# Performance work log

Measured on AMD Instinct MI355X. Metric: run time of the kernel, lower is better.

The kernel has to match this reference:

```python
import jax, jax.numpy as jnp
import numpy as np

B, N, K = 64, 128, 12
D_ATOM, D_NBR, D_NEW = 256, 320, 256
H, DK = 8, 32  # D_NEW = H * DK
LN_EPS = 1e-5
NEG_INF = -1e9


def setup_inputs() -> dict:
    key = jax.random.key(0)
    ks = jax.random.split(key, 10)
    atom_feature = jax.random.normal(ks[0], (B, N, D_ATOM), jnp.float32)
    atom_neighbor_feature = jax.random.normal(ks[1], (B, N, K, D_NBR), jnp.float32)
    # valid-neighbor masks from random neighbor counts in [1, K]
    counts = jax.random.randint(ks[2], (B, N), 1, K + 1)
    valid = (jnp.arange(K)[None, None, :] < counts[:, :, None]).astype(jnp.float32)
    atom_attend_mask = valid[..., None]                      # (B,N,K,1), 1=real neighbor
    atom_softmax_mask = (1.0 - valid[..., None]) * NEG_INF   # (B,N,K,1), additive
    # parameters
    s = 1.0 / np.sqrt(D_ATOM)
    W_atom = jax.random.uniform(ks[3], (D_ATOM, D_NEW), jnp.float32, -s, s)
    b_atom = jnp.zeros((D_NEW,), jnp.float32)
    s2 = 1.0 / np.sqrt(D_NBR)
    W_nbr = jax.random.uniform(ks[4], (D_NBR, D_NEW), jnp.float32, -s2, s2)
    b_nbr = jnp.zeros((D_NEW,), jnp.float32)
    s3 = 1.0 / np.sqrt(DK)
    w_align = jax.random.uniform(ks[5], (DK, 1), jnp.float32, -s3, s3)
    b_align = jnp.zeros((1,), jnp.float32)
    ln_gamma = jnp.ones((D_NEW,), jnp.float32)
    ln_beta = jnp.zeros((D_NEW,), jnp.float32)
    return dict(atom_feature=atom_feature, atom_neighbor_feature=atom_neighbor_feature,
                atom_softmax_mask=atom_softmax_mask, atom_attend_mask=atom_attend_mask,
                W_atom=W_atom, b_atom=b_atom, W_nbr=W_nbr, b_nbr=b_nbr,
                w_align=w_align, b_align=b_align, ln_gamma=ln_gamma, ln_beta=ln_beta)


def reference(atom_feature, atom_neighbor_feature, atom_softmax_mask, atom_attend_mask,
              W_atom, b_atom, W_nbr, b_nbr, w_align, b_align, ln_gamma, ln_beta):
    # dropout is identity at eval time
    h = atom_feature @ W_atom + b_atom                    # (B,N,D_NEW)
    e = atom_neighbor_feature @ W_nbr + b_nbr             # (B,N,K,D_NEW)
    h = h.reshape(B, N, 1, H, DK)                         # broadcast over K
    e = e.reshape(B, N, K, H, DK)
    # GATv2: act(h_i + e_j) then per-head linear score
    feat = jax.nn.leaky_relu(h + e)                       # slope 0.01 == torch default
    score = feat @ w_align + b_align                      # (B,N,K,H,1)
    score = score + atom_softmax_mask[:, :, :, None, :]   # additive -inf on pad
    attn = jax.nn.softmax(score, axis=2)                  # softmax over neighbors K
    attn = attn * atom_attend_mask[:, :, :, None, :]
    ctx = jnp.sum(attn * e, axis=2).reshape(B, N, H * DK)  # (B,N,D_NEW)
    # LayerNorm
    mu = jnp.mean(ctx, axis=-1, keepdims=True)
    xc = ctx - mu
    var = jnp.mean(xc * xc, axis=-1, keepdims=True)
    return xc * jax.lax.rsqrt(var + LN_EPS) * ln_gamma + ln_beta
```

## Files before the change

kernel.cpp:

```cpp
#include <hip/hip_runtime.h>

#define KN 12
#define DNBR 320
#define DNEW 256
#define BN_TOT 8192
#define ATB 2
#define NKS_E 10
#define NKS_H 8
#define ASTR_E 328
#define ASTR_H 264

typedef short bf8_t __attribute__((ext_vector_type(8)));
typedef float f32x4 __attribute__((ext_vector_type(4)));
typedef unsigned short us8 __attribute__((ext_vector_type(8)));
using u16 = unsigned short;
using u32 = unsigned int;

__device__ __forceinline__ u16 f2bf(float f) {
    u32 x = __float_as_uint(f);
    return (u16)((x + 0x7fffu + ((x >> 16) & 1u)) >> 16);
}

__device__ __forceinline__ us8 pack8(float4 a, float4 b) {
    us8 v;
    v[0] = f2bf(a.x); v[1] = f2bf(a.y); v[2] = f2bf(a.z); v[3] = f2bf(a.w);
    v[4] = f2bf(b.x); v[5] = f2bf(b.y); v[6] = f2bf(b.z); v[7] = f2bf(b.w);
    return v;
}

__global__ __launch_bounds__(256) void build_b2(
    const float* __restrict__ Wn, const float* __restrict__ Wa,
    u16* __restrict__ B2)
{
    int tile = blockIdx.x * 4 + (threadIdx.x >> 6);
    int l = threadIdx.x & 63;
    int q = l >> 4, m = l & 15;
    us8 v;
    if (tile < 160) {
        int ks = tile >> 4, nt = tile & 15;
        int col = nt * 16 + m;
#pragma unroll
        for (int e = 0; e < 8; e++)
            v[e] = f2bf(Wn[(ks * 32 + q * 8 + e) * DNEW + col]);
    } else {
        int tt = tile - 160;
        int ks = tt >> 4, nt = tt & 15;
        int col = nt * 16 + m;
#pragma unroll
        for (int e = 0; e < 8; e++)
            v[e] = f2bf(Wa[(ks * 32 + q * 8 + e) * DNEW + col]);
    }
    *(us8*)&B2[(size_t)tile * 512 + l * 8] = v;
}

__global__ __launch_bounds__(256, 4) void fused_all(
    const float* __restrict__ atomf, const float* __restrict__ nbrf,
    const float* __restrict__ smaskg, const float* __restrict__ amaskg,
    const float* __restrict__ ba, const u16* __restrict__ B2,
    const float* __restrict__ bnb, const float* __restrict__ walg,
    const float* __restrict__ balg, const float* __restrict__ gam,
    const float* __restrict__ bet, float* __restrict__ out)
{
    __shared__ u16 A_e[32 * ASTR_E];
    __shared__ u16 A_h[16 * ASTR_H];
    __shared__ float h_l[ATB][256];
    __shared__ float ctx_l[ATB][256];
    __shared__ float s_l[ATB][8][12];
    __shared__ float attnm_l[ATB][8][16];
    __shared__ float bnb_l[256], ba_l[256], wal_l[32];
    __shared__ float smask_l[ATB * 12], amask_l[ATB * 12];
    __shared__ float red_l[ATB][8];

    const int t = threadIdx.x;
    const int l = t & 63, w = t >> 6, q = l >> 4, m = l & 15;
    const int a0 = blockIdx.x * ATB;

    bnb_l[t] = bnb[t];
    ba_l[t] = ba[t];
    if (t < 32) wal_l[t] = walg[t];
    else if (t >= 32 && t < 56) smask_l[t - 32] = smaskg[(size_t)a0 * KN + (t - 32)];
    else if (t >= 64 && t < 88) amask_l[t - 64] = amaskg[(size_t)a0 * KN + (t - 64)];

    const float* nbase = nbrf + (size_t)a0 * (KN * DNBR);
    for (int i = t; i < 960; i += 256) {
        float4 v0 = *(const float4*)(nbase + i * 8);
        float4 v1 = *(const float4*)(nbase + i * 8 + 4);
        int at = i / 480, rem = i - at * 480;
        int row = rem / 40, c8 = rem - row * 40;
        *(us8*)&A_e[(at * 16 + row) * ASTR_E + c8 * 8] = pack8(v0, v1);
    }
    for (int i = t; i < 328; i += 256) {
        int at = i / 164, rem = i - at * 164;
        int rr = rem / 41, c8 = rem - rr * 41;
        us8 z = {0, 0, 0, 0, 0, 0, 0, 0};
        *(us8*)&A_e[(at * 16 + 12 + rr) * ASTR_E + c8 * 8] = z;
    }
    if (t < 64) {
        int at = t >> 5, c8 = t & 31;
        const float* s = atomf + (size_t)(a0 + at) * DNEW + c8 * 8;
        *(us8*)&A_h[at * ASTR_H + c8 * 8] = pack8(*(const float4*)s, *(const float4*)(s + 4));
    }
    for (int i = t; i < 462; i += 256) {
        int rr = i / 33, c8 = i - rr * 33;
        us8 z = {0, 0, 0, 0, 0, 0, 0, 0};
        *(us8*)&A_h[(2 + rr) * ASTR_H + c8 * 8] = z;
    }
    __syncthreads();

    f32x4 acc_e[ATB][4];
    f32x4 acc_h[4];
#pragma unroll
    for (int at = 0; at < ATB; at++)
#pragma unroll
        for (int j = 0; j < 4; j++) acc_e[at][j] = (f32x4){0.f, 0.f, 0.f, 0.f};
#pragma unroll
    for (int j = 0; j < 4; j++) acc_h[j] = (f32x4){0.f, 0.f, 0.f, 0.f};

    for (int ks = 0; ks < NKS_E; ks++) {
        bf8_t af0 = *(bf8_t*)&A_e[(0 * 16 + m) * ASTR_E + ks * 32 + q * 8];
        bf8_t af1 = *(bf8_t*)&A_e[(1 * 16 + m) * ASTR_E + ks * 32 + q * 8];
        bf8_t bf[4];
#pragma unroll
        for (int j = 0; j < 4; j++)
            bf[j] = *(const bf8_t*)&B2[((size_t)(ks * 16 + w * 4 + j) * 64 + l) * 8];
#pragma unroll
        for (int j = 0; j < 4; j++) {
            acc_e[0][j] = __builtin_amdgcn_mfma_f32_16x16x32_bf16(af0, bf[j], acc_e[0][j], 0, 0, 0);
            acc_e[1][j] = __builtin_amdgcn_mfma_f32_16x16x32_bf16(af1, bf[j], acc_e[1][j], 0, 0, 0);
        }
    }
    for (int ks = 0; ks < NKS_H; ks++) {
        bf8_t af = *(bf8_t*)&A_h[m * ASTR_H + ks * 32 + q * 8];
#pragma unroll
        for (int j = 0; j < 4; j++) {
            bf8_t bfj = *(const bf8_t*)&B2[((size_t)(160 + ks * 16 + w * 4 + j) * 64 + l) * 8];
            acc_h[j] = __builtin_amdgcn_mfma_f32_16x16x32_bf16(af, bfj, acc_h[j], 0, 0, 0);
        }
    }
    if (q == 0) {
#pragma unroll
        for (int j = 0; j < 4; j++) {
            int col = w * 64 + j * 16 + m;
            h_l[0][col] = acc_h[j][0] + ba_l[col];
            h_l[1][col] = acc_h[j][1] + ba_l[col];
        }
    }
    __syncthreads();

#pragma unroll
    for (int j = 0; j < 4; j++) {
        float bv = bnb_l[w * 64 + j * 16 + m];
#pragma unroll
        for (int at = 0; at < ATB; at++)
#pragma unroll
            for (int r = 0; r < 4; r++) acc_e[at][j][r] += bv;
    }

    const float bal = balg[0];
    float hv[ATB][4], wv[4];
#pragma unroll
    for (int j = 0; j < 4; j++) {
        wv[j] = wal_l[(j * 16 + m) & 31];
#pragma unroll
        for (int at = 0; at < ATB; at++) hv[at][j] = h_l[at][w * 64 + j * 16 + m];
    }
#pragma unroll
    for (int at = 0; at < ATB; at++) {
#pragma unroll
        for (int jj = 0; jj < 2; jj++) {
#pragma unroll
            for (int r = 0; r < 4; r++) {
                float p = 0.f;
#pragma unroll
                for (int jo = 0; jo < 2; jo++) {
                    int j = jj * 2 + jo;
                    float f = acc_e[at][j][r] + hv[at][j];
                    f = f > 0.f ? f : 0.01f * f;
                    p = fmaf(f, wv[j], p);
                }
                p += __shfl_xor(p, 1);
                p += __shfl_xor(p, 2);
                p += __shfl_xor(p, 4);
                p += __shfl_xor(p, 8);
                int k = q * 4 + r;
                if (m == 0 && k < 12)
                    s_l[at][w * 2 + jj][k] = p + bal + smask_l[at * 12 + k];
            }
        }
    }
    __syncthreads();

    if (t < ATB * 8) {
        int at = t >> 3, hd = t & 7;
        float sc[12], mx = -1e30f;
#pragma unroll
        for (int k = 0; k < 12; k++) { sc[k] = s_l[at][hd][k]; mx = fmaxf(mx, sc[k]); }
        float ss = 0.f;
#pragma unroll
        for (int k = 0; k < 12; k++) { sc[k] = __expf(sc[k] - mx); ss += sc[k]; }
        float inv = 1.f / ss;
#pragma unroll
        for (int k = 0; k < 12; k++)
            attnm_l[at][hd][k] = sc[k] * inv * amask_l[at * 12 + k];
        attnm_l[at][hd][12] = 0.f;
        attnm_l[at][hd][13] = 0.f;
        attnm_l[at][hd][14] = 0.f;
        attnm_l[at][hd][15] = 0.f;
    }
    __syncthreads();

#pragma unroll
    for (int at = 0; at < ATB; at++) {
#pragma unroll
        for (int j = 0; j < 4; j++) {
            int hd = w * 2 + (j >> 1);
            f32x4 am = *(f32x4*)&attnm_l[at][hd][q * 4];
            float cp = am[0] * acc_e[at][j][0] + am[1] * acc_e[at][j][1] +
                       am[2] * acc_e[at][j][2] + am[3] * acc_e[at][j][3];
            cp += __shfl_xor(cp, 16);
            cp += __shfl_xor(cp, 32);
            if (q == 0) ctx_l[at][w * 64 + j * 16 + m] = cp;
        }
    }
    __syncthreads();

    float x[ATB];
#pragma unroll
    for (int at = 0; at < ATB; at++) {
        x[at] = ctx_l[at][t];
        float s1 = x[at], s2 = x[at] * x[at];
#pragma unroll
        for (int off = 1; off < 64; off <<= 1) {
            s1 += __shfl_xor(s1, off);
            s2 += __shfl_xor(s2, off);
        }
        if (l == 0) { red_l[at][w] = s1; red_l[at][4 + w] = s2; }
    }
    __syncthreads();
#pragma unroll
    for (int at = 0; at < ATB; at++) {
        float ts1 = red_l[at][0] + red_l[at][1] + red_l[at][2] + red_l[at][3];
        float ts2 = red_l[at][4] + red_l[at][5] + red_l[at][6] + red_l[at][7];
        float mu = ts1 * (1.f / 256.f);
        float var = ts2 * (1.f / 256.f) - mu * mu;
        var = fmaxf(var, 0.f);
        float r = rsqrtf(var + 1e-5f);
        out[(size_t)(a0 + at) * DNEW + t] = (x[at] - mu) * r * gam[t] + bet[t];
    }
}

extern "C" void kernel_launch(void* const* d_in, const int* in_sizes, int n_in,
                              void* d_out, int out_size, void* d_ws, size_t ws_size,
                              hipStream_t stream) {
    const float* atomf = (const float*)d_in[0];
    const float* nbrf  = (const float*)d_in[1];
    const float* smask = (const float*)d_in[2];
    const float* amask = (const float*)d_in[3];
    const float* Wa    = (const float*)d_in[4];
    const float* ba    = (const float*)d_in[5];
    const float* Wn    = (const float*)d_in[6];
    const float* bnb   = (const float*)d_in[7];
    const float* wal   = (const float*)d_in[8];
    const float* bal   = (const float*)d_in[9];
    const float* gam   = (const float*)d_in[10];
    const float* bet   = (const float*)d_in[11];
    float* outp = (float*)d_out;

    u16* B2 = (u16*)d_ws;

    build_b2<<<72, 256, 0, stream>>>(Wn, Wa, B2);
    fused_all<<<BN_TOT / ATB, 256, 0, stream>>>(atomf, nbrf, smask, amask, ba,
                                                B2, bnb, wal, bal, gam, bet, outp);
}
```

Baseline: 266.3 us.

## Split atom projection into separate kernel and do softmax/LayerNorm in registers

Moves the atom-feature projection h into a separate pre-kernel that batches 32 atoms per block and writes h to workspace. The main kernel no longer pads h to a 16-row MFMA tile, which wasted most of that work. It also packs both atoms' 12 neighbor rows into 28 LDS rows instead of 32, and runs the softmax, context reduction and LayerNorm statistics in registers with shuffles, dropping several LDS buffers and barriers. Lower LDS use and launch bounds of 6 aim at higher occupancy, at the cost of an extra launch and an h round-trip through global memory.

```diff
diff --git a/kernel.cpp b/kernel.cpp
--- a/kernel.cpp
+++ b/kernel.cpp
@@ -9,6 +9,7 @@
 #define NKS_H 8
 #define ASTR_E 328
 #define ASTR_H 264
+#define H_OFF 294912
 
 typedef short bf8_t __attribute__((ext_vector_type(8)));
 typedef float f32x4 __attribute__((ext_vector_type(4)));
@@ -53,22 +54,68 @@
     *(us8*)&B2[(size_t)tile * 512 + l * 8] = v;
 }
 
-__global__ __launch_bounds__(256, 4) void fused_all(
-    const float* __restrict__ atomf, const float* __restrict__ nbrf,
+__global__ __launch_bounds__(256) void h_pre(
+    const float* __restrict__ atomf, const u16* __restrict__ B2,
+    const float* __restrict__ ba, float* __restrict__ h_g)
+{
+    __shared__ u16 A[32 * ASTR_H];
+
+    const int t = threadIdx.x;
+    const int l = t & 63, w = t >> 6, q = l >> 4, m = l & 15;
+    const int ab = blockIdx.x * 32;
+
+    const float* base = atomf + (size_t)ab * DNEW;
+    for (int i = t; i < 1024; i += 256) {
+        float4 v0 = *(const float4*)(base + i * 8);
+        float4 v1 = *(const float4*)(base + i * 8 + 4);
+        int a = i >> 5, c8 = i & 31;
+        *(us8*)&A[a * ASTR_H + c8 * 8] = pack8(v0, v1);
+    }
+    __syncthreads();
+
+    f32x4 acc[2][4];
+#pragma unroll
+    for (int mt = 0; mt < 2; mt++)
+#pragma unroll
+        for (int j = 0; j < 4; j++) acc[mt][j] = (f32x4){0.f, 0.f, 0.f, 0.f};
+
+    for (int ks = 0; ks < NKS_H; ks++) {
+        bf8_t af0 = *(bf8_t*)&A[m * ASTR_H + ks * 32 + q * 8];
+        bf8_t af1 = *(bf8_t*)&A[(16 + m) * ASTR_H + ks * 32 + q * 8];
+#pragma unroll
+        for (int j = 0; j < 4; j++) {
+            bf8_t bfj = *(const bf8_t*)&B2[((size_t)(160 + ks * 16 + w * 4 + j) * 64 + l) * 8];
+            acc[0][j] = __builtin_amdgcn_mfma_f32_16x16x32_bf16(af0, bfj, acc[0][j], 0, 0, 0);
+            acc[1][j] = __builtin_amdgcn_mfma_f32_16x16x32_bf16(af1, bfj, acc[1][j], 0, 0, 0);
+        }
+    }
+#pragma unroll
+    for (int mt = 0; mt < 2; mt++)
+#pragma unroll
+        for (int j = 0; j < 4; j++) {
+            int col = w * 64 + j * 16 + m;
+            float bav = ba[col];
+#pragma unroll
+            for (int r = 0; r < 4; r++) {
+                int row = ab + mt * 16 + q * 4 + r;
+                h_g[(size_t)row * DNEW + col] = acc[mt][j][r] + bav;
+            }
+        }
+}
+
+__global__ __launch_bounds__(256, 6) void fused_all(
+    const float* __restrict__ nbrf,
     const float* __restrict__ smaskg, const float* __restrict__ amaskg,
-    const float* __restrict__ ba, const u16* __restrict__ B2,
+    const u16* __restrict__ B2, const float* __restrict__ h_g,
     const float* __restrict__ bnb, const float* __restrict__ walg,
     const float* __restrict__ balg, const float* __restrict__ gam,
     const float* __restrict__ bet, float* __restrict__ out)
 {
-    __shared__ u16 A_e[32 * ASTR_E];
-    __shared__ u16 A_h[16 * ASTR_H];
-    __shared__ float h_l[ATB][256];
-    __shared__ float ctx_l[ATB][256];
-    __shared__ float s_l[ATB][8][12];
-    __shared__ float attnm_l[ATB][8][16];
-    __shared__ float bnb_l[256], ba_l[256], wal_l[32];
-    __shared__ float smask_l[ATB * 12], amask_l[ATB * 12];
+    __shared__ u16 A_e[28 * ASTR_E];
+    __shared__ float bnb_l[256];
+    __shared__ float wal_l[32];
+    __shared__ float smask_l[ATB * KN];
+    __shared__ float amask_l[ATB * KN];
     __shared__ float red_l[ATB][8];
 
     const int t = threadIdx.x;
@@ -76,10 +123,11 @@
     const int a0 = blockIdx.x * ATB;
 
     bnb_l[t] = bnb[t];
-    ba_l[t] = ba[t];
     if (t < 32) wal_l[t] = walg[t];
-    else if (t >= 32 && t < 56) smask_l[t - 32] = smaskg[(size_t)a0 * KN + (t - 32)];
-    else if (t >= 64 && t < 88) amask_l[t - 64] = amaskg[(size_t)a0 * KN + (t - 64)];
+    else if (t >= 32 && t < 32 + ATB * KN)
+        smask_l[t - 32] = smaskg[(size_t)a0 * KN + (t - 32)] + balg[0];
+    else if (t >= 64 && t < 64 + ATB * KN)
+        amask_l[t - 64] = amaskg[(size_t)a0 * KN + (t - 64)];
 
     const float* nbase = nbrf + (size_t)a0 * (KN * DNBR);
     for (int i = t; i < 960; i += 256) {
@@ -87,65 +135,40 @@
         float4 v1 = *(const float4*)(nbase + i * 8 + 4);
         int at = i / 480, rem = i - at * 480;
         int row = rem / 40, c8 = rem - row * 40;
-        *(us8*)&A_e[(at * 16 + row) * ASTR_E + c8 * 8] = pack8(v0, v1);
-    }
-    for (int i = t; i < 328; i += 256) {
-        int at = i / 164, rem = i - at * 164;
-        int rr = rem / 41, c8 = rem - rr * 41;
+        *(us8*)&A_e[(at * 12 + row) * ASTR_E + c8 * 8] = pack8(v0, v1);
+    }
+    if (t < 164) {
+        int rr = t / 41, c8 = t - rr * 41;
         us8 z = {0, 0, 0, 0, 0, 0, 0, 0};
-        *(us8*)&A_e[(at * 16 + 12 + rr) * ASTR_E + c8 * 8] = z;
-    }
-    if (t < 64) {
-        int at = t >> 5, c8 = t & 31;
-        const float* s = atomf + (size_t)(a0 + at) * DNEW + c8 * 8;
-        *(us8*)&A_h[at * ASTR_H + c8 * 8] = pack8(*(const float4*)s, *(const float4*)(s + 4));
-    }
-    for (int i = t; i < 462; i += 256) {
-        int rr = i / 33, c8 = i - rr * 33;
-        us8 z = {0, 0, 0, 0, 0, 0, 0, 0};
-        *(us8*)&A_h[(2 + rr) * ASTR_H + c8 * 8] = z;
-    }
+        *(us8*)&A_e[(24 + rr) * ASTR_E + c8 * 8] = z;
+    }
+
+    float hv[ATB][4];
+#pragma unroll
+    for (int j = 0; j < 4; j++) {
+        int col = w * 64 + j * 16 + m;
+        hv[0][j] = h_g[(size_t)(a0 + 0) * DNEW + col];
+        hv[1][j] = h_g[(size_t)(a0 + 1) * DNEW + col];
+    }
+
     __syncthreads();
 
     f32x4 acc_e[ATB][4];
-    f32x4 acc_h[4];
 #pragma unroll
     for (int at = 0; at < ATB; at++)
 #pragma unroll
         for (int j = 0; j < 4; j++) acc_e[at][j] = (f32x4){0.f, 0.f, 0.f, 0.f};
-#pragma unroll
-    for (int j = 0; j < 4; j++) acc_h[j] = (f32x4){0.f, 0.f, 0.f, 0.f};
 
     for (int ks = 0; ks < NKS_E; ks++) {
-        bf8_t af0 = *(bf8_t*)&A_e[(0 * 16 + m) * ASTR_E + ks * 32 + q * 8];
-        bf8_t af1 = *(bf8_t*)&A_e[(1 * 16 + m) * ASTR_E + ks * 32 + q * 8];
-        bf8_t bf[4];
-#pragma unroll
-        for (int j = 0; j < 4; j++)
-            bf[j] = *(const bf8_t*)&B2[((size_t)(ks * 16 + w * 4 + j) * 64 + l) * 8];
+        bf8_t af0 = *(bf8_t*)&A_e[m * ASTR_E + ks * 32 + q * 8];
+        bf8_t af1 = *(bf8_t*)&A_e[(12 + m) * ASTR_E + ks * 32 + q * 8];
 #pragma unroll
         for (int j = 0; j < 4; j++) {
-            acc_e[0][j] = __builtin_amdgcn_mfma_f32_16x16x32_bf16(af0, bf[j], acc_e[0][j], 0, 0, 0);
-            acc_e[1][j] = __builtin_amdgcn_mfma_f32_16x16x32_bf16(af1, bf[j], acc_e[1][j], 0, 0, 0);
-        }
-    }
-    for (int ks = 0; ks < NKS_H; ks++) {
-        bf8_t af = *(bf8_t*)&A_h[m * ASTR_H + ks * 32 + q * 8];
-#pragma unroll
-        for (int j = 0; j < 4; j++) {
-            bf8_t bfj = *(const bf8_t*)&B2[((size_t)(160 + ks * 16 + w * 4 + j) * 64 + l) * 8];
-            acc_h[j] = __builtin_amdgcn_mfma_f32_16x16x32_bf16(af, bfj, acc_h[j], 0, 0, 0);
-        }
-    }
-    if (q == 0) {
-#pragma unroll
-        for (int j = 0; j < 4; j++) {
-            int col = w * 64 + j * 16 + m;
-            h_l[0][col] = acc_h[j][0] + ba_l[col];
-            h_l[1][col] = acc_h[j][1] + ba_l[col];
-        }
-    }
-    __syncthreads();
+            bf8_t bfj = *(const bf8_t*)&B2[((size_t)(ks * 16 + w * 4 + j) * 64 + l) * 8];
+            acc_e[0][j] = __builtin_amdgcn_mfma_f32_16x16x32_bf16(af0, bfj, acc_e[0][j], 0, 0, 0);
+            acc_e[1][j] = __builtin_amdgcn_mfma_f32_16x16x32_bf16(af1, bfj, acc_e[1][j], 0, 0, 0);
+        }
+    }
 
 #pragma unroll
     for (int j = 0; j < 4; j++) {
@@ -156,87 +179,70 @@
             for (int r = 0; r < 4; r++) acc_e[at][j][r] += bv;
     }
 
-    const float bal = balg[0];
-    float hv[ATB][4], wv[4];
-#pragma unroll
-    for (int j = 0; j < 4; j++) {
-        wv[j] = wal_l[(j * 16 + m) & 31];
-#pragma unroll
-        for (int at = 0; at < ATB; at++) hv[at][j] = h_l[at][w * 64 + j * 16 + m];
-    }
+    float wv[4];
+#pragma unroll
+    for (int j = 0; j < 4; j++) wv[j] = wal_l[(j * 16 + m) & 31];
+
+    float ctxv[ATB][4];
 #pragma unroll
     for (int at = 0; at < ATB; at++) {
+        float s1 = 0.f, s2 = 0.f;
 #pragma unroll
         for (int jj = 0; jj < 2; jj++) {
+            float p[4];
 #pragma unroll
             for (int r = 0; r < 4; r++) {
-                float p = 0.f;
+                float pp = 0.f;
 #pragma unroll
                 for (int jo = 0; jo < 2; jo++) {
                     int j = jj * 2 + jo;
                     float f = acc_e[at][j][r] + hv[at][j];
                     f = f > 0.f ? f : 0.01f * f;
-                    p = fmaf(f, wv[j], p);
+                    pp = fmaf(f, wv[j], pp);
                 }
-                p += __shfl_xor(p, 1);
-                p += __shfl_xor(p, 2);
-                p += __shfl_xor(p, 4);
-                p += __shfl_xor(p, 8);
-                int k = q * 4 + r;
-                if (m == 0 && k < 12)
-                    s_l[at][w * 2 + jj][k] = p + bal + smask_l[at * 12 + k];
-            }
-        }
-    }
-    __syncthreads();
-
-    if (t < ATB * 8) {
-        int at = t >> 3, hd = t & 7;
-        float sc[12], mx = -1e30f;
-#pragma unroll
-        for (int k = 0; k < 12; k++) { sc[k] = s_l[at][hd][k]; mx = fmaxf(mx, sc[k]); }
-        float ss = 0.f;
-#pragma unroll
-        for (int k = 0; k < 12; k++) { sc[k] = __expf(sc[k] - mx); ss += sc[k]; }
-        float inv = 1.f / ss;
-#pragma unroll
-        for (int k = 0; k < 12; k++)
-            attnm_l[at][hd][k] = sc[k] * inv * amask_l[at * 12 + k];
-        attnm_l[at][hd][12] = 0.f;
-        attnm_l[at][hd][13] = 0.f;
-        attnm_l[at][hd][14] = 0.f;
-        attnm_l[at][hd][15] = 0.f;
-    }
-    __syncthreads();
-
-#pragma unroll
-    for (int at = 0; at < ATB; at++) {
-#pragma unroll
-        for (int j = 0; j < 4; j++) {
-            int hd = w * 2 + (j >> 1);
-            f32x4 am = *(f32x4*)&attnm_l[at][hd][q * 4];
-            float cp = am[0] * acc_e[at][j][0] + am[1] * acc_e[at][j][1] +
-                       am[2] * acc_e[at][j][2] + am[3] * acc_e[at][j][3];
-            cp += __shfl_xor(cp, 16);
-            cp += __shfl_xor(cp, 32);
-            if (q == 0) ctx_l[at][w * 64 + j * 16 + m] = cp;
-        }
-    }
-    __syncthreads();
-
-    float x[ATB];
-#pragma unroll
-    for (int at = 0; at < ATB; at++) {
-        x[at] = ctx_l[at][t];
-        float s1 = x[at], s2 = x[at] * x[at];
-#pragma unroll
-        for (int off = 1; off < 64; off <<= 1) {
+                pp += __shfl_xor(pp, 1);
+                pp += __shfl_xor(pp, 2);
+                pp += __shfl_xor(pp, 4);
+                pp += __shfl_xor(pp, 8);
+                p[r] = (q < 3) ? pp + smask_l[at * KN + q * 4 + r] : -1e30f;
+            }
+            float mx = fmaxf(fmaxf(p[0], p[1]), fmaxf(p[2], p[3]));
+            mx = fmaxf(mx, __shfl_xor(mx, 16));
+            mx = fmaxf(mx, __shfl_xor(mx, 32));
+            float ex[4], ss = 0.f;
+#pragma unroll
+            for (int r = 0; r < 4; r++) {
+                ex[r] = (q < 3) ? __expf(p[r] - mx) : 0.f;
+                ss += ex[r];
+            }
+            ss += __shfl_xor(ss, 16);
+            ss += __shfl_xor(ss, 32);
+            float inv = 1.f / ss;
+            float am[4];
+#pragma unroll
+            for (int r = 0; r < 4; r++)
+                am[r] = (q < 3) ? ex[r] * inv * amask_l[at * KN + q * 4 + r] : 0.f;
+#pragma unroll
+            for (int jo = 0; jo < 2; jo++) {
+                int j = jj * 2 + jo;
+                float cp = am[0] * acc_e[at][j][0] + am[1] * acc_e[at][j][1] +
+                           am[2] * acc_e[at][j][2] + am[3] * acc_e[at][j][3];
+                cp += __shfl_xor(cp, 16);
+                cp += __shfl_xor(cp, 32);
+                ctxv[at][j] = cp;
+                s1 += cp;
+                s2 += cp * cp;
+            }
+        }
+#pragma unroll
+        for (int off = 1; off < 16; off <<= 1) {
             s1 += __shfl_xor(s1, off);
             s2 += __shfl_xor(s2, off);
         }
         if (l == 0) { red_l[at][w] = s1; red_l[at][4 + w] = s2; }
     }
     __syncthreads();
+
 #pragma unroll
     for (int at = 0; at < ATB; at++) {
         float ts1 = red_l[at][0] + red_l[at][1] + red_l[at][2] + red_l[at][3];
@@ -244,8 +250,15 @@
         float mu = ts1 * (1.f / 256.f);
         float var = ts2 * (1.f / 256.f) - mu * mu;
         var = fmaxf(var, 0.f);
-        float r = rsqrtf(var + 1e-5f);
-        out[(size_t)(a0 + at) * DNEW + t] = (x[at] - mu) * r * gam[t] + bet[t];
+        float rs = rsqrtf(var + 1e-5f);
+        if (q == 0) {
+#pragma unroll
+            for (int j = 0; j < 4; j++) {
+                int col = w * 64 + j * 16 + m;
+                out[(size_t)(a0 + at) * DNEW + col] =
+                    (ctxv[at][j] - mu) * rs * gam[col] + bet[col];
+            }
+        }
     }
 }
 
@@ -267,8 +280,10 @@
     float* outp = (float*)d_out;
 
     u16* B2 = (u16*)d_ws;
+    float* h_g = (float*)((char*)d_ws + H_OFF);
 
     build_b2<<<72, 256, 0, stream>>>(Wn, Wa, B2);
-    fused_all<<<BN_TOT / ATB, 256, 0, stream>>>(atomf, nbrf, smask, amask, ba,
-                                                B2, bnb, wal, bal, gam, bet, outp);
-}
+    h_pre<<<BN_TOT / 32, 256, 0, stream>>>(atomf, B2, ba, h_g);
+    fused_all<<<BN_TOT / ATB, 256, 0, stream>>>(nbrf, smask, amask, B2, h_g,
+                                                bnb, wal, bal, gam, bet, outp);
+}
```

After: 265.3 us. Within noise of the previous version (-0.4%).
